# Kernel optimization log

Hardware: AMD Instinct MI355X
Metric: run time of the kernel (lower is better)

Reference implementation:

```python
import jax, jax.numpy as jnp
import numpy as np

# dims: B batch, N seq, D model_dim, R lora rank, C codebooks, K codebook_input_channel, P kv pairs, M per-codebook output
B, N, D, R, C, K, P = 4, 2048, 1024, 8, 64, 16, 64
M = (D * R) // C  # 128


def setup_inputs() -> dict:
    key = jax.random.key(0)
    ks = jax.random.split(key, 7)
    x = jax.random.normal(ks[0], (B, N, D), dtype=jnp.float32)
    W_A = jax.random.normal(ks[1], (C, K, D), dtype=jnp.float32) * (D ** -0.5)
    emb_A = jax.random.uniform(ks[2], (C, P, K), dtype=jnp.float32, minval=-1.5, maxval=1.5)
    vals_A = jax.random.normal(ks[3], (C, P, M), dtype=jnp.float32)
    W_B = jax.random.normal(ks[4], (C, K, D), dtype=jnp.float32) * (D ** -0.5)
    emb_B = jax.random.uniform(ks[5], (C, P, K), dtype=jnp.float32, minval=-1.5, maxval=1.5)
    vals_B = jax.random.normal(ks[6], (C, P, M), dtype=jnp.float32)
    return {"x": x, "W_A": W_A, "emb_A": emb_A, "vals_A": vals_A,
            "W_B": W_B, "emb_B": emb_B, "vals_B": vals_B}


def _discrete_kv(x, W, emb, vals):
    # x: [B,N,D]; W: [C,K,D] (Linear weight per codebook); emb: [C,P,K]; vals: [C,P,M]
    proj = jnp.einsum('bnd,ckd->cbnk', x, W)  # per-codebook linear projection
    # squared euclidean distance to each key (argmin is same as cdist argmin)
    d2 = (jnp.sum(proj * proj, axis=-1, keepdims=True)
          - 2.0 * jnp.einsum('cbnk,cpk->cbnp', proj, emb)
          + jnp.sum(emb * emb, axis=-1)[:, None, None, :])  # [C,B,N,P]
    idx = jnp.argmin(d2, axis=-1)                      # [C,B,N]
    y = jax.vmap(lambda v, i: v[i])(vals, idx)          # [C,B,N,M]
    # concat over codebooks on last dim -> [B,N,C*M], then view as [B,N,R,D]
    return jnp.transpose(y, (1, 2, 0, 3)).reshape(x.shape[0], x.shape[1], R, D)


def reference(x, W_A, emb_A, vals_A, W_B, emb_B, vals_B):
    A = _discrete_kv(x, W_A, emb_A, vals_A)   # [B,N,R,D]
    Bm = _discrete_kv(x, W_B, emb_B, vals_B)  # [B,N,R,D]
    t = jnp.einsum('bnd,bnrd->bnr', x, A)
    return jnp.einsum('bnr,bnrd->bnd', t, Bm)
```

## Files before the change

### kernel.cpp

```cpp
#include <hip/hip_runtime.h>

#define NTOK   8192
#define DMODEL 1024
#define NC     64
#define NK     16
#define NP     64
#define NM     128
#define LCAP   (1 << 18)
#define MARGIN 2e-3f

typedef _Float16 f16x8 __attribute__((ext_vector_type(8)));
typedef float    f32x4 __attribute__((ext_vector_type(4)));

#define AS1 __attribute__((address_space(1)))
#define AS3 __attribute__((address_space(3)))

__device__ __forceinline__ void glds16(const void* g, void* l) {
    __builtin_amdgcn_global_load_lds((const AS1 void*)g, (AS3 void*)l, 16, 0, 0);
}

__global__ __launch_bounds__(256) void k_split(
    const float* __restrict__ x, const float* __restrict__ W_A, const float* __restrict__ W_B,
    short* __restrict__ xh, short* __restrict__ xl,
    short* __restrict__ whA, short* __restrict__ wlA,
    short* __restrict__ whB, short* __restrict__ wlB)
{
    const int t = blockIdx.x * 256 + threadIdx.x;
    const int NX = 128 * NTOK;
    const int NW = 128 * 1024;

    const float* src;
    short *dh, *dl;
    if (t < NX) {
        const int chunk = t >> 13, tok = t & 8191;
        src = x + (size_t)tok * DMODEL + chunk * 8;
        dh = xh + (size_t)t * 8;  dl = xl + (size_t)t * 8;
    } else if (t < NX + NW) {
        const int u = t - NX, chunk = u >> 10, ck = u & 1023;
        src = W_A + (size_t)ck * DMODEL + chunk * 8;
        dh = whA + (size_t)u * 8; dl = wlA + (size_t)u * 8;
    } else {
        const int u = t - NX - NW, chunk = u >> 10, ck = u & 1023;
        src = W_B + (size_t)ck * DMODEL + chunk * 8;
        dh = whB + (size_t)u * 8; dl = wlB + (size_t)u * 8;
    }

    const float4 a = *(const float4*)src;
    const float4 b = *(const float4*)(src + 4);
    const float v[8] = {a.x, a.y, a.z, a.w, b.x, b.y, b.z, b.w};
    unsigned h[8], l[8];
    #pragma unroll
    for (int j = 0; j < 8; ++j) {
        const _Float16 hf = (_Float16)v[j];
        const _Float16 lf = (_Float16)(v[j] - (float)hf);
        h[j] = (unsigned)__builtin_bit_cast(unsigned short, hf);
        l[j] = (unsigned)__builtin_bit_cast(unsigned short, lf);
    }
    *(int4*)dh = make_int4((int)(h[0] | (h[1] << 16)), (int)(h[2] | (h[3] << 16)),
                           (int)(h[4] | (h[5] << 16)), (int)(h[6] | (h[7] << 16)));
    *(int4*)dl = make_int4((int)(l[0] | (l[1] << 16)), (int)(l[2] | (l[3] << 16)),
                           (int)(l[4] | (l[5] << 16)), (int)(l[6] | (l[7] << 16)));
}

__global__ __launch_bounds__(256, 2) void k_mfma_argmin(
    const short* __restrict__ xh, const short* __restrict__ xl,
    const short* __restrict__ whA, const short* __restrict__ wlA,
    const short* __restrict__ whB, const short* __restrict__ wlB,
    const float* __restrict__ emb_A, const float* __restrict__ emb_B,
    int* __restrict__ idxbuf, int* __restrict__ list, int* __restrict__ cnt)
{
    __shared__ __align__(16) float smem[16384];
    short* ls = (short*)smem;
    float* proj = smem;
    float* embS = smem + 8448;
    float* e2S  = smem + 12576;

    const int tid = threadIdx.x;
    const int bid = blockIdx.x;
    const int swz = (bid & 7) * 128 + (bid >> 3);
    const int tb  = swz >> 4;
    const int ot  = swz & 15;
    const int set = ot >> 3;
    const short* __restrict__ wh = set ? whB : whA;
    const short* __restrict__ wl = set ? wlB : wlA;
    const float* __restrict__ Ep = set ? emb_B : emb_A;
    const int cbase = (ot & 7) * 8;

    const int lane = tid & 63;
    const int wid  = tid >> 6;
    const int wr   = wid >> 1;
    const int wc   = wid & 1;
    const int lrow = lane & 15;
    const int lk   = lane >> 4;

    f32x4 acc[4][4];
    #pragma unroll
    for (int m = 0; m < 4; ++m)
        #pragma unroll
        for (int n = 0; n < 4; ++n) acc[m][n] = (f32x4){0.f, 0.f, 0.f, 0.f};

    const int r7 = tid >> 7, r127 = tid & 127;
    const short* gA0 = xh + ((size_t)r7 * NTOK + tb * 128 + r127) * 8;
    const short* gA1 = xl + ((size_t)r7 * NTOK + tb * 128 + r127) * 8;
    const short* gB0 = wh + ((size_t)r7 * 1024 + cbase * 16 + r127) * 8;
    const short* gB1 = wl + ((size_t)r7 * 1024 + cbase * 16 + r127) * 8;

    #define STAGE(buf, st)                                                   \
        do {                                                                 \
            const size_t sa_ = (size_t)(st) * (4 * NTOK * 8);                \
            const size_t sb_ = (size_t)(st) * (4 * 1024 * 8);                \
            short* lb_ = ls + (buf) * 16384 + tid * 8;                       \
            glds16(gA0 + sa_,                lb_);                           \
            glds16(gA0 + sa_ + 2 * NTOK * 8, lb_ + 2048);                    \
            glds16(gA1 + sa_,                lb_ + 4096);                    \
            glds16(gA1 + sa_ + 2 * NTOK * 8, lb_ + 6144);                    \
            glds16(gB0 + sb_,                lb_ + 8192);                    \
            glds16(gB0 + sb_ + 2 * 1024 * 8, lb_ + 10240);                   \
            glds16(gB1 + sb_,                lb_ + 12288);                   \
            glds16(gB1 + sb_ + 2 * 1024 * 8, lb_ + 14336);                   \
        } while (0)

    const int fa = (lk * 128 + wr * 64 + lrow) * 8;
    const int fb = 8192 + (lk * 128 + wc * 64 + lrow) * 8;

    STAGE(0, 0);
    for (int t = 0; t < 32; ++t) {
        const int cur = t & 1;
        if (t < 31) {
            STAGE(cur ^ 1, t + 1);
            asm volatile("s_waitcnt vmcnt(8)" ::: "memory");
        } else {
            asm volatile("s_waitcnt vmcnt(0)" ::: "memory");
        }
        __builtin_amdgcn_sched_barrier(0);
        __builtin_amdgcn_s_barrier();

        const short* pa = ls + cur * 16384 + fa;
        const short* pb = ls + cur * 16384 + fb;
        f16x8 ah[4], al[4], bh[4], bl[4];
        #pragma unroll
        for (int m = 0; m < 4; ++m) {
            ah[m] = *(const f16x8*)(pa + m * 128);
            al[m] = *(const f16x8*)(pa + 4096 + m * 128);
            bh[m] = *(const f16x8*)(pb + m * 128);
            bl[m] = *(const f16x8*)(pb + 4096 + m * 128);
        }
        #pragma unroll
        for (int m = 0; m < 4; ++m)
            #pragma unroll
            for (int n = 0; n < 4; ++n) {
                acc[m][n] = __builtin_amdgcn_mfma_f32_16x16x32_f16(ah[m], bh[n], acc[m][n], 0, 0, 0);
                acc[m][n] = __builtin_amdgcn_mfma_f32_16x16x32_f16(ah[m], bl[n], acc[m][n], 0, 0, 0);
                acc[m][n] = __builtin_amdgcn_mfma_f32_16x16x32_f16(al[m], bh[n], acc[m][n], 0, 0, 0);
            }
        __builtin_amdgcn_s_barrier();
    }
    #undef STAGE

    for (int h = 0; h < 2; ++h) {
        __syncthreads();
        if (wr == h) {
            #pragma unroll
            for (int m = 0; m < 4; ++m)
                #pragma unroll
                for (int n = 0; n < 4; ++n)
                    #pragma unroll
                    for (int r = 0; r < 4; ++r)
                        proj[(m * 16 + lk * 4 + r) * 132 + wc * 64 + n * 16 + lrow] = acc[m][n][r];
        }
        for (int ch = 0; ch < 2; ++ch) {
            __syncthreads();
            {
                const float4* eg = (const float4*)(Ep + (size_t)(cbase + ch * 4) * NP * NK);
                #pragma unroll
                for (int i = 0; i < 4; ++i) {
                    const int idx = tid + 256 * i;
                    const int cb4 = idx >> 8, win = idx & 255;
                    ((float4*)(embS + cb4 * 1032))[win] = eg[idx];
                }
            }
            __syncthreads();
            {
                const float* e = embS + (tid >> 6) * 1032 + (tid & 63) * 16;
                float s = 0.f;
                #pragma unroll
                for (int k = 0; k < 16; ++k) s = fmaf(e[k], e[k], s);
                e2S[tid] = s;
            }
            __syncthreads();
            {
                const int cl = tid >> 6, lt = tid & 63;
                float pr[16];
                const float4* pp = (const float4*)(proj + lt * 132 + (ch * 4 + cl) * 16);
                #pragma unroll
                for (int q = 0; q < 4; ++q) {
                    const float4 v = pp[q];
                    pr[q * 4 + 0] = v.x; pr[q * 4 + 1] = v.y;
                    pr[q * 4 + 2] = v.z; pr[q * 4 + 3] = v.w;
                }
                const float4* eb4 = (const float4*)(embS + cl * 1032);
                const float* e2 = e2S + cl * 64;
                float best = 1e30f, second = 1e30f;
                int bp = 0;
                for (int p = 0; p < 64; ++p) {
                    const float4 e0 = eb4[p * 4 + 0], e1 = eb4[p * 4 + 1];
                    const float4 e2v = eb4[p * 4 + 2], e3 = eb4[p * 4 + 3];
                    float s = 0.f;
                    s = fmaf(pr[0], e0.x, s);   s = fmaf(pr[1], e0.y, s);
                    s = fmaf(pr[2], e0.z, s);   s = fmaf(pr[3], e0.w, s);
                    s = fmaf(pr[4], e1.x, s);   s = fmaf(pr[5], e1.y, s);
                    s = fmaf(pr[6], e1.z, s);   s = fmaf(pr[7], e1.w, s);
                    s = fmaf(pr[8], e2v.x, s);  s = fmaf(pr[9], e2v.y, s);
                    s = fmaf(pr[10], e2v.z, s); s = fmaf(pr[11], e2v.w, s);
                    s = fmaf(pr[12], e3.x, s);  s = fmaf(pr[13], e3.y, s);
                    s = fmaf(pr[14], e3.z, s);  s = fmaf(pr[15], e3.w, s);
                    const float g = fmaf(-2.f, s, e2[p]);
                    if (g < best) { second = best; best = g; bp = p; }
                    else if (g < second) { second = g; }
                }
                const int c = cbase + ch * 4 + cl;
                const int gtok = tb * 128 + h * 64 + lt;
                idxbuf[(set * NC + c) * NTOK + gtok] = bp;
                if (second - best < MARGIN) {
                    const int slot = atomicAdd(cnt, 1);
                    if (slot < LCAP) list[slot] = (set << 19) | (c << 13) | gtok;
                }
            }
        }
    }
}

__global__ __launch_bounds__(256) void k_refine(
    const float* __restrict__ x,
    const float* __restrict__ W_A, const float* __restrict__ W_B,
    const float* __restrict__ emb_A, const float* __restrict__ emb_B,
    const int* __restrict__ list, const int* __restrict__ cnt,
    int* __restrict__ idxbuf)
{
    int n = *cnt;
    if (n > LCAP) n = LCAP;
    const int lane = threadIdx.x & 63;
    const int wave = (int)((blockIdx.x * blockDim.x + threadIdx.x) >> 6);
    const int nw   = (int)((gridDim.x * blockDim.x) >> 6);

    for (int i = wave; i < n; i += nw) {
        const int code = list[i];
        const int tok = code & 8191;
        const int c   = (code >> 13) & 63;
        const int set = (code >> 19) & 1;
        const float* __restrict__ Wp = set ? W_B : W_A;
        const float* __restrict__ Ep = set ? emb_B : emb_A;

        double pk[16];
        #pragma unroll
        for (int k = 0; k < 16; ++k) pk[k] = 0.0;
        for (int dd = 0; dd < 16; ++dd) {
            const int d = dd * 64 + lane;
            const double xv = (double)x[(size_t)tok * DMODEL + d];
            #pragma unroll
            for (int k = 0; k < 16; ++k)
                pk[k] = fma(xv, (double)Wp[(size_t)(c * 16 + k) * DMODEL + d], pk[k]);
        }
        #pragma unroll
        for (int k = 0; k < 16; ++k) {
            #pragma unroll
            for (int off = 32; off; off >>= 1)
                pk[k] += __shfl_xor(pk[k], off, 64);
        }
        double d2 = 0.0;
        #pragma unroll
        for (int k = 0; k < 16; ++k) {
            const double t = pk[k] - (double)Ep[(size_t)(c * NP + lane) * NK + k];
            d2 = fma(t, t, d2);
        }
        int bp = lane;
        double bv = d2;
        #pragma unroll
        for (int off = 32; off; off >>= 1) {
            const double ov = __shfl_xor(bv, off, 64);
            const int    op = __shfl_xor(bp, off, 64);
            if (ov < bv || (ov == bv && op < bp)) { bv = ov; bp = op; }
        }
        if (lane == 0) idxbuf[(set * NC + c) * NTOK + tok] = bp;
    }
}

__global__ __launch_bounds__(256) void k_combine(
    const float* __restrict__ x,
    const float* __restrict__ vals_A, const float* __restrict__ vals_B,
    const int* __restrict__ idxbuf, float* __restrict__ out)
{
    __shared__ float xsh[1032];
    __shared__ float part[256];
    __shared__ float tsh[8];
    __shared__ int sIA[64];
    __shared__ int sIB[64];

    const int tid = threadIdx.x;
    const int tok = blockIdx.x;

    if (tid < 64) {
        sIA[tid] = idxbuf[tid * NTOK + tok];
        sIB[tid] = idxbuf[(NC + tid) * NTOK + tok];
    }
    {
        const float4 v = *(const float4*)(x + (size_t)tok * DMODEL + tid * 4);
        const int base = tid * 4 + (tid >> 5);
        xsh[base + 0] = v.x;
        xsh[base + 1] = v.y;
        xsh[base + 2] = v.z;
        xsh[base + 3] = v.w;
    }
    __syncthreads();
    {
        const int c = tid & 63, mseg = tid >> 6;
        const int ia = sIA[c];
        const float4* va = (const float4*)(vals_A + (size_t)(c * NP + ia) * NM + mseg * 32);
        const float* xb = xsh + (c & 7) * 129 + mseg * 32;
        float s = 0.f;
        #pragma unroll
        for (int i = 0; i < 8; ++i) {
            const float4 v = va[i];
            s = fmaf(v.x, xb[i * 4 + 0], s);
            s = fmaf(v.y, xb[i * 4 + 1], s);
            s = fmaf(v.z, xb[i * 4 + 2], s);
            s = fmaf(v.w, xb[i * 4 + 3], s);
        }
        part[tid] = s;
    }
    __syncthreads();
    if (tid < 8) {
        float s = 0.f;
        #pragma unroll
        for (int m = 0; m < 4; ++m)
            #pragma unroll
            for (int j = 0; j < 8; ++j)
                s += part[m * 64 + tid * 8 + j];
        tsh[tid] = s;
    }
    __syncthreads();
    {
        const int d0 = tid * 4, dblk = tid >> 5, dm = d0 & 127;
        float o0 = 0.f, o1 = 0.f, o2 = 0.f, o3 = 0.f;
        #pragma unroll
        for (int r = 0; r < 8; ++r) {
            const int cb = 8 * r + dblk;
            const int ib = sIB[cb];
            const float4 v = *(const float4*)(vals_B + (size_t)(cb * NP + ib) * NM + dm);
            const float tv = tsh[r];
            o0 = fmaf(tv, v.x, o0);
            o1 = fmaf(tv, v.y, o1);
            o2 = fmaf(tv, v.z, o2);
            o3 = fmaf(tv, v.w, o3);
        }
        *(float4*)(out + (size_t)tok * DMODEL + d0) = make_float4(o0, o1, o2, o3);
    }
}

extern "C" void kernel_launch(void* const* d_in, const int* in_sizes, int n_in,
                              void* d_out, int out_size, void* d_ws, size_t ws_size,
                              hipStream_t stream)
{
    const float* x      = (const float*)d_in[0];
    const float* W_A    = (const float*)d_in[1];
    const float* emb_A  = (const float*)d_in[2];
    const float* vals_A = (const float*)d_in[3];
    const float* W_B    = (const float*)d_in[4];
    const float* emb_B  = (const float*)d_in[5];
    const float* vals_B = (const float*)d_in[6];
    float* out = (float*)d_out;

    char* w = (char*)d_ws;
    int*   cnt    = (int*)w;
    int*   list   = (int*)(w + 16);
    int*   idxbuf = (int*)(w + 16 + sizeof(int) * (size_t)LCAP);
    size_t off = 16 + sizeof(int) * (size_t)LCAP + sizeof(int) * (size_t)(2 * NC * NTOK);
    short* xh  = (short*)(w + off); off += (size_t)NTOK * DMODEL * 2;
    short* xl  = (short*)(w + off); off += (size_t)NTOK * DMODEL * 2;
    short* whA = (short*)(w + off); off += (size_t)1024 * DMODEL * 2;
    short* wlA = (short*)(w + off); off += (size_t)1024 * DMODEL * 2;
    short* whB = (short*)(w + off); off += (size_t)1024 * DMODEL * 2;
    short* wlB = (short*)(w + off);

    hipMemsetAsync(cnt, 0, sizeof(int), stream);
    k_split<<<5120, 256, 0, stream>>>(x, W_A, W_B, xh, xl, whA, wlA, whB, wlB);
    k_mfma_argmin<<<1024, 256, 0, stream>>>(xh, xl, whA, wlA, whB, wlB,
                                            emb_A, emb_B, idxbuf, list, cnt);
    k_refine<<<1024, 256, 0, stream>>>(x, W_A, W_B, emb_A, emb_B, list, cnt, idxbuf);
    k_combine<<<NTOK, 256, 0, stream>>>(x, vals_A, vals_B, idxbuf, out);
}
```

Baseline: 234.4 us.

## Enlarge projection GEMM tile to 256x256 with 32x32 MFMA and 512 threads

The split-fp16 projection GEMM moves from 128x128 tiles on 256-thread blocks to 256x256 tiles on 512-thread blocks, and swaps 16x16x32 MFMA for 32x32x16 MFMA. The goal is more reuse of each LDS load per FLOP and less global traffic, since each block now covers more tokens and more codebook channels. The argmin epilogue is reorganised to match, with a transposed projection buffer and codebook embeddings staged eight at a time. In exchange the grid shrinks to 256 blocks at one block per CU, with double the LDS footprint, which lowers occupancy and reduces latency hiding.

```diff
diff --git a/kernel.cpp b/kernel.cpp
--- a/kernel.cpp
+++ b/kernel.cpp
@@ -9,8 +9,8 @@
 #define LCAP   (1 << 18)
 #define MARGIN 2e-3f
 
-typedef _Float16 f16x8 __attribute__((ext_vector_type(8)));
-typedef float    f32x4 __attribute__((ext_vector_type(4)));
+typedef _Float16 f16x8  __attribute__((ext_vector_type(8)));
+typedef float    f32x16 __attribute__((ext_vector_type(16)));
 
 #define AS1 __attribute__((address_space(1)))
 #define AS3 __attribute__((address_space(3)))
@@ -62,66 +62,64 @@
                            (int)(l[4] | (l[5] << 16)), (int)(l[6] | (l[7] << 16)));
 }
 
-__global__ __launch_bounds__(256, 2) void k_mfma_argmin(
+__global__ __launch_bounds__(512, 1) void k_mfma_argmin(
     const short* __restrict__ xh, const short* __restrict__ xl,
     const short* __restrict__ whA, const short* __restrict__ wlA,
     const short* __restrict__ whB, const short* __restrict__ wlB,
     const float* __restrict__ emb_A, const float* __restrict__ emb_B,
     int* __restrict__ idxbuf, int* __restrict__ list, int* __restrict__ cnt)
 {
-    __shared__ __align__(16) float smem[16384];
+    __shared__ __align__(16) float smem[32768];
     short* ls = (short*)smem;
-    float* proj = smem;
-    float* embS = smem + 8448;
-    float* e2S  = smem + 12576;
+    float* projT = smem;
+    float* embS  = smem + 16640;
+    float* e2S   = smem + 24832;
 
     const int tid = threadIdx.x;
     const int bid = blockIdx.x;
-    const int swz = (bid & 7) * 128 + (bid >> 3);
-    const int tb  = swz >> 4;
-    const int ot  = swz & 15;
-    const int set = ot >> 3;
+    const int swz = (bid & 7) * 32 + (bid >> 3);
+    const int tb  = swz >> 3;
+    const int ot  = swz & 7;
+    const int set = ot >> 2;
     const short* __restrict__ wh = set ? whB : whA;
     const short* __restrict__ wl = set ? wlB : wlA;
     const float* __restrict__ Ep = set ? emb_B : emb_A;
-    const int cbase = (ot & 7) * 8;
+    const int ckbase = (ot & 3) * 256;
 
     const int lane = tid & 63;
     const int wid  = tid >> 6;
-    const int wr   = wid >> 1;
-    const int wc   = wid & 1;
-    const int lrow = lane & 15;
-    const int lk   = lane >> 4;
-
-    f32x4 acc[4][4];
+    const int wr   = wid >> 2;
+    const int wc   = wid & 3;
+    const int lr31 = lane & 31;
+    const int lk2  = lane >> 5;
+
+    f32x16 acc[4][2];
     #pragma unroll
     for (int m = 0; m < 4; ++m)
         #pragma unroll
-        for (int n = 0; n < 4; ++n) acc[m][n] = (f32x4){0.f, 0.f, 0.f, 0.f};
-
-    const int r7 = tid >> 7, r127 = tid & 127;
-    const short* gA0 = xh + ((size_t)r7 * NTOK + tb * 128 + r127) * 8;
-    const short* gA1 = xl + ((size_t)r7 * NTOK + tb * 128 + r127) * 8;
-    const short* gB0 = wh + ((size_t)r7 * 1024 + cbase * 16 + r127) * 8;
-    const short* gB1 = wl + ((size_t)r7 * 1024 + cbase * 16 + r127) * 8;
+        for (int n = 0; n < 2; ++n)
+            #pragma unroll
+            for (int r = 0; r < 16; ++r) acc[m][n][r] = 0.f;
+
+    const size_t oA0 = ((size_t)(tid >> 8) * NTOK + tb * 256 + (tid & 255)) * 8;
+    const size_t oA1 = ((size_t)((tid + 512) >> 8) * NTOK + tb * 256 + (tid & 255)) * 8;
+    const size_t oB0 = ((size_t)(tid >> 8) * 1024 + ckbase + (tid & 255)) * 8;
+    const size_t oB1 = ((size_t)((tid + 512) >> 8) * 1024 + ckbase + (tid & 255)) * 8;
 
     #define STAGE(buf, st)                                                   \
         do {                                                                 \
             const size_t sa_ = (size_t)(st) * (4 * NTOK * 8);                \
             const size_t sb_ = (size_t)(st) * (4 * 1024 * 8);                \
-            short* lb_ = ls + (buf) * 16384 + tid * 8;                       \
-            glds16(gA0 + sa_,                lb_);                           \
-            glds16(gA0 + sa_ + 2 * NTOK * 8, lb_ + 2048);                    \
-            glds16(gA1 + sa_,                lb_ + 4096);                    \
-            glds16(gA1 + sa_ + 2 * NTOK * 8, lb_ + 6144);                    \
-            glds16(gB0 + sb_,                lb_ + 8192);                    \
-            glds16(gB0 + sb_ + 2 * 1024 * 8, lb_ + 10240);                   \
-            glds16(gB1 + sb_,                lb_ + 12288);                   \
-            glds16(gB1 + sb_ + 2 * 1024 * 8, lb_ + 14336);                   \
+            short* lb_ = ls + (buf) * 32768 + tid * 8;                       \
+            glds16(xh + oA0 + sa_, lb_);                                     \
+            glds16(xh + oA1 + sa_, lb_ + 4096);                              \
+            glds16(xl + oA0 + sa_, lb_ + 8192);                              \
+            glds16(xl + oA1 + sa_, lb_ + 12288);                             \
+            glds16(wh + oB0 + sb_, lb_ + 16384);                             \
+            glds16(wh + oB1 + sb_, lb_ + 20480);                             \
+            glds16(wl + oB0 + sb_, lb_ + 24576);                             \
+            glds16(wl + oB1 + sb_, lb_ + 28672);                             \
         } while (0)
-
-    const int fa = (lk * 128 + wr * 64 + lrow) * 8;
-    const int fb = 8192 + (lk * 128 + wc * 64 + lrow) * 8;
 
     STAGE(0, 0);
     for (int t = 0; t < 32; ++t) {
@@ -135,71 +133,80 @@
         __builtin_amdgcn_sched_barrier(0);
         __builtin_amdgcn_s_barrier();
 
-        const short* pa = ls + cur * 16384 + fa;
-        const short* pb = ls + cur * 16384 + fb;
-        f16x8 ah[4], al[4], bh[4], bl[4];
-        #pragma unroll
-        for (int m = 0; m < 4; ++m) {
-            ah[m] = *(const f16x8*)(pa + m * 128);
-            al[m] = *(const f16x8*)(pa + 4096 + m * 128);
-            bh[m] = *(const f16x8*)(pb + m * 128);
-            bl[m] = *(const f16x8*)(pb + 4096 + m * 128);
-        }
-        #pragma unroll
-        for (int m = 0; m < 4; ++m)
-            #pragma unroll
-            for (int n = 0; n < 4; ++n) {
-                acc[m][n] = __builtin_amdgcn_mfma_f32_16x16x32_f16(ah[m], bh[n], acc[m][n], 0, 0, 0);
-                acc[m][n] = __builtin_amdgcn_mfma_f32_16x16x32_f16(ah[m], bl[n], acc[m][n], 0, 0, 0);
-                acc[m][n] = __builtin_amdgcn_mfma_f32_16x16x32_f16(al[m], bh[n], acc[m][n], 0, 0, 0);
+        const short* pbuf = ls + cur * 32768;
+        #pragma unroll
+        for (int ks = 0; ks < 2; ++ks) {
+            const int kc2 = ks * 2 + lk2;
+            const short* pa = pbuf + (kc2 * 256 + wr * 128 + lr31) * 8;
+            const short* pB = pbuf + 16384 + (kc2 * 256 + wc * 64 + lr31) * 8;
+            f16x8 ah[4], al[4], bh[2], bl[2];
+            #pragma unroll
+            for (int m = 0; m < 4; ++m) {
+                ah[m] = *(const f16x8*)(pa + m * 256);
+                al[m] = *(const f16x8*)(pa + 8192 + m * 256);
             }
-        __builtin_amdgcn_s_barrier();
-    }
-    #undef STAGE
-
-    for (int h = 0; h < 2; ++h) {
-        __syncthreads();
-        if (wr == h) {
+            #pragma unroll
+            for (int n = 0; n < 2; ++n) {
+                bh[n] = *(const f16x8*)(pB + n * 256);
+                bl[n] = *(const f16x8*)(pB + 8192 + n * 256);
+            }
             #pragma unroll
             for (int m = 0; m < 4; ++m)
                 #pragma unroll
-                for (int n = 0; n < 4; ++n)
+                for (int n = 0; n < 2; ++n) {
+                    acc[m][n] = __builtin_amdgcn_mfma_f32_32x32x16_f16(ah[m], bh[n], acc[m][n], 0, 0, 0);
+                    acc[m][n] = __builtin_amdgcn_mfma_f32_32x32x16_f16(ah[m], bl[n], acc[m][n], 0, 0, 0);
+                    acc[m][n] = __builtin_amdgcn_mfma_f32_32x32x16_f16(al[m], bh[n], acc[m][n], 0, 0, 0);
+                }
+        }
+        __builtin_amdgcn_s_barrier();
+    }
+    #undef STAGE
+
+    #pragma unroll
+    for (int ch = 0; ch < 2; ++ch) {
+        __syncthreads();
+        {
+            const float4* eg = (const float4*)(Ep + (size_t)((ot & 3) * 16 + ch * 8) * NP * NK);
+            float4* es = (float4*)embS;
+            #pragma unroll
+            for (int i = 0; i < 4; ++i) es[tid + 512 * i] = eg[tid + 512 * i];
+        }
+        __syncthreads();
+        {
+            const float* e = embS + tid * 16;
+            float s = 0.f;
+            #pragma unroll
+            for (int k = 0; k < 16; ++k) s = fmaf(e[k], e[k], s);
+            e2S[tid] = s;
+        }
+        #pragma unroll
+        for (int c = 0; c < 4; ++c) {
+            __syncthreads();
+            if (wr == (c >> 1)) {
+                #pragma unroll
+                for (int mi = 0; mi < 2; ++mi) {
+                    const int m = (c & 1) * 2 + mi;
                     #pragma unroll
-                    for (int r = 0; r < 4; ++r)
-                        proj[(m * 16 + lk * 4 + r) * 132 + wc * 64 + n * 16 + lrow] = acc[m][n][r];
-        }
-        for (int ch = 0; ch < 2; ++ch) {
-            __syncthreads();
-            {
-                const float4* eg = (const float4*)(Ep + (size_t)(cbase + ch * 4) * NP * NK);
-                #pragma unroll
-                for (int i = 0; i < 4; ++i) {
-                    const int idx = tid + 256 * i;
-                    const int cb4 = idx >> 8, win = idx & 255;
-                    ((float4*)(embS + cb4 * 1032))[win] = eg[idx];
+                    for (int n = 0; n < 2; ++n) {
+                        const int col = wc * 64 + n * 32 + lr31;
+                        #pragma unroll
+                        for (int r = 0; r < 16; ++r) {
+                            const int trow = mi * 32 + (r & 3) + 8 * (r >> 2) + 4 * lk2;
+                            projT[col * 65 + trow] = acc[m][n][r];
+                        }
+                    }
                 }
             }
             __syncthreads();
             {
-                const float* e = embS + (tid >> 6) * 1032 + (tid & 63) * 16;
-                float s = 0.f;
+                const int lt = tid & 63, cbl = tid >> 6;
+                float pr[16];
                 #pragma unroll
-                for (int k = 0; k < 16; ++k) s = fmaf(e[k], e[k], s);
-                e2S[tid] = s;
-            }
-            __syncthreads();
-            {
-                const int cl = tid >> 6, lt = tid & 63;
-                float pr[16];
-                const float4* pp = (const float4*)(proj + lt * 132 + (ch * 4 + cl) * 16);
-                #pragma unroll
-                for (int q = 0; q < 4; ++q) {
-                    const float4 v = pp[q];
-                    pr[q * 4 + 0] = v.x; pr[q * 4 + 1] = v.y;
-                    pr[q * 4 + 2] = v.z; pr[q * 4 + 3] = v.w;
-                }
-                const float4* eb4 = (const float4*)(embS + cl * 1032);
-                const float* e2 = e2S + cl * 64;
+                for (int k = 0; k < 16; ++k)
+                    pr[k] = projT[((ch * 8 + cbl) * 16 + k) * 65 + lt];
+                const float4* eb4 = (const float4*)(embS + cbl * 1024);
+                const float* e2 = e2S + cbl * 64;
                 float best = 1e30f, second = 1e30f;
                 int bp = 0;
                 for (int p = 0; p < 64; ++p) {
@@ -218,12 +225,12 @@
                     if (g < best) { second = best; best = g; bp = p; }
                     else if (g < second) { second = g; }
                 }
-                const int c = cbase + ch * 4 + cl;
-                const int gtok = tb * 128 + h * 64 + lt;
-                idxbuf[(set * NC + c) * NTOK + gtok] = bp;
+                const int cbook = (ot & 3) * 16 + ch * 8 + cbl;
+                const int gtok = tb * 256 + c * 64 + lt;
+                idxbuf[(set * NC + cbook) * NTOK + gtok] = bp;
                 if (second - best < MARGIN) {
                     const int slot = atomicAdd(cnt, 1);
-                    if (slot < LCAP) list[slot] = (set << 19) | (c << 13) | gtok;
+                    if (slot < LCAP) list[slot] = (set << 19) | (cbook << 13) | gtok;
                 }
             }
         }
@@ -384,8 +391,8 @@
 
     hipMemsetAsync(cnt, 0, sizeof(int), stream);
     k_split<<<5120, 256, 0, stream>>>(x, W_A, W_B, xh, xl, whA, wlA, whB, wlB);
-    k_mfma_argmin<<<1024, 256, 0, stream>>>(xh, xl, whA, wlA, whB, wlB,
-                                            emb_A, emb_B, idxbuf, list, cnt);
+    k_mfma_argmin<<<256, 512, 0, stream>>>(xh, xl, whA, wlA, whB, wlB,
+                                           emb_A, emb_B, idxbuf, list, cnt);
     k_refine<<<1024, 256, 0, stream>>>(x, W_A, W_B, emb_A, emb_B, list, cnt, idxbuf);
     k_combine<<<NTOK, 256, 0, stream>>>(x, vals_A, vals_B, idxbuf, out);
 }
```

Measured after the change: 242.0 us. +3.3%, slower.
